# Performance work log

Measured on AMD Instinct MI355X. Metric: run time of the kernel, lower is better.

## Reference

```python
import jax, jax.numpy as jnp
import numpy as np

NGF = 64
EPS = 1e-5


def _rpad(x):
    # ReflectionPad2d(1)
    return jnp.pad(x, ((0, 0), (0, 0), (1, 1), (1, 1)), mode='reflect')


def _inorm(x):
    # InstanceNorm2d(affine=False): per-sample, per-channel over H,W
    m = x.mean(axis=(2, 3), keepdims=True)
    v = ((x - m) ** 2).mean(axis=(2, 3), keepdims=True)
    return (x - m) / jnp.sqrt(v + EPS)


def _pac_conv(xp, gp, w, b):
    # Pixel-adaptive conv (pac.PacConv2d, kernel_type='gaussian', k=3, pad=0).
    # xp: (B,C,H+2,W+2) padded input; gp: (B,Cg,H+2,W+2) padded guide;
    # w: (O,C,3,3), b: (O,)
    B, C, Hp, Wp = xp.shape
    H, W = Hp - 2, Wp - 2
    gc = gp[:, :, 1:1 + H, 1:1 + W]  # guide value at each output pixel (patch center)
    out = jnp.zeros((B, w.shape[0], H, W), xp.dtype)
    for ky in range(3):
        for kx in range(3):
            gs = gp[:, :, ky:ky + H, kx:kx + W]
            # Gaussian adaptive kernel: exp(-0.5 * ||g_nb - g_center||^2), summed over guide channels
            k = jnp.exp(-0.5 * jnp.sum((gs - gc) ** 2, axis=1, keepdims=True))  # (B,1,H,W)
            xs = xp[:, :, ky:ky + H, kx:kx + W] * k
            out = out + jnp.einsum('oc,bchw->bohw', w[:, :, ky, kx], xs)
    return out + b[None, :, None, None]


def _pa_resblock(h, guide, wa, ba, wb, bb):
    gp = _rpad(guide)
    t = h
    h = _pac_conv(_rpad(h), gp, wa, ba)
    h = jax.nn.relu(_inorm(h))
    h = _pac_conv(_rpad(h), gp, wb, bb)
    h = _inorm(h)
    return t + h


def setup_inputs() -> dict:
    key = jax.random.key(0)
    ks = jax.random.split(key, 20)
    B, Cin, H, W = 4, 1, 256, 256
    d = {
        'x': jax.random.normal(ks[0], (B, Cin, H, W), jnp.float32),
        'grad_img': jax.random.normal(ks[1], (B, Cin, H, W), jnp.float32),
        'w0': jax.random.normal(ks[2], (NGF, Cin, 1, 1), jnp.float32) * 0.5,
        'b0': jnp.zeros((NGF,), jnp.float32),
        'wf': jax.random.normal(ks[3], (NGF, NGF, 3, 3), jnp.float32) * 0.05,
        'bf': jnp.zeros((NGF,), jnp.float32),
    }
    for i in (1, 2, 3):
        d[f'w{i}a'] = jax.random.normal(ks[3 + 2 * i], (NGF, NGF, 3, 3), jnp.float32) * 0.05
        d[f'b{i}a'] = jnp.zeros((NGF,), jnp.float32)
        d[f'w{i}b'] = jax.random.normal(ks[4 + 2 * i], (NGF, NGF, 3, 3), jnp.float32) * 0.05
        d[f'b{i}b'] = jnp.zeros((NGF,), jnp.float32)
    return d


def reference(x, grad_img, w0, b0, wf, bf,
              w1a, b1a, w1b, b1b,
              w2a, b2a, w2b, b2b,
              w3a, b3a, w3b, b3b):
    # type == 'ir': y = minmax(grad_img) is computed but unused; guide = x
    guide = x
    # 1x1 stem conv
    h = jnp.einsum('oc,bchw->bohw', w0[:, :, 0, 0], x) + b0[None, :, None, None]
    h = jax.nn.relu(_pa_resblock(h, guide, w1a, b1a, w1b, b1b))
    h = jax.nn.relu(_pa_resblock(h, guide, w2a, b2a, w2b, b2b))
    h = jax.nn.relu(_pa_resblock(h, guide, w3a, b3a, w3b, b3b))
    # model2: reflect pad + 3x3 conv + relu
    hp = _rpad(h)
    out = jax.lax.conv_general_dilated(
        hp, wf, window_strides=(1, 1), padding='VALID',
        dimension_numbers=('NCHW', 'OIHW', 'NCHW'))
    out = jax.nn.relu(out + bf[None, :, None, None])
    return out
```

## Files before the change

kernel.cpp:

```cpp
#include <hip/hip_runtime.h>
#include <hip/hip_bf16.h>
#include <math.h>

#define BN 4
#define CHN 64
#define HH 256
#define WW 256
#define HWSZ (HH*WW)
#define EPSV 1e-5f
#define CP 72

typedef __attribute__((ext_vector_type(8)))  short  short8;
typedef __attribute__((ext_vector_type(4)))  short  short4v;
typedef __attribute__((ext_vector_type(16))) float  floatx16;

__device__ __forceinline__ int refl(int i, int n){ if(i<0)i=-i; if(i>=n)i=2*n-2-i; return i; }
__device__ __forceinline__ short f2bf(float f){ __hip_bfloat16 h=__float2bfloat16(f); return __builtin_bit_cast(short,h); }
__device__ __forceinline__ float bf2f(short s){ unsigned u=((unsigned)(unsigned short)s)<<16; return __builtin_bit_cast(float,u); }

template<int CTRL>
__device__ __forceinline__ float dpp_add(float x){
    int y = __builtin_amdgcn_update_dpp(0, __builtin_bit_cast(int, x), CTRL, 0xF, 0xF, true);
    return x + __builtin_bit_cast(float, y);
}
__device__ __forceinline__ float red_cols(float x){
    x = dpp_add<0xB1>(x);
    x = dpp_add<0x4E>(x);
    x = dpp_add<0x124>(x);
    x = dpp_add<0x128>(x);
    x = dpp_add<0x142>(x);
    return x;
}

__global__ void guide_kernel(const float* __restrict__ x, float* __restrict__ Kb) {
    int idx = blockIdx.x * 256 + threadIdx.x;
    if (idx >= BN*HWSZ) return;
    int b = idx / HWSZ, p = idx - b*HWSZ;
    int y = p / WW, xx = p - y*WW;
    const float* g = x + b*HWSZ;
    float gc = g[p];
#pragma unroll
    for (int t = 0; t < 9; ++t) {
        int yy  = refl(y + t/3 - 1, HH);
        int xx2 = refl(xx + t%3 - 1, WW);
        float d = g[yy*WW + xx2] - gc;
        Kb[(b*9 + t)*HWSZ + p] = __expf(-0.5f*d*d);
    }
}

__global__ void pack_all(const float* w1,const float* w2,const float* w3,const float* w4,
                         const float* w5,const float* w6,const float* w7, short* __restrict__ Ap){
    const float* wsrc[7] = {w1,w2,w3,w4,w5,w6,w7};
    int layer = blockIdx.y;
    int tid = blockIdx.x*256 + threadIdx.x;
    int j    = tid & 7;
    int lane = (tid >> 3) & 63;
    int frag = tid >> 9;
    int oh = frag & 1, cg = (frag >> 1) & 3, t = frag >> 3;
    int o = oh*32 + (lane & 31);
    int c = cg*16 + (lane >> 5)*8 + j;
    Ap[(size_t)layer*36864 + tid] = f2bf(wsrc[layer][(o*CHN + c)*9 + t]);
}

__global__ void conv1x1_kernel(const float* __restrict__ x, const float* __restrict__ w0,
                               const float* __restrict__ b0, short* __restrict__ A){
    int idx = blockIdx.x*256 + threadIdx.x;
    int oc = idx & 7;
    int px = (idx >> 3) % HWSZ;
    int b  = idx / (HWSZ*8);
    float xv = x[(size_t)b*HWSZ + px];
    short8 r;
#pragma unroll
    for (int j = 0; j < 8; ++j) {
        int c = oc*8 + j;
        r[j] = f2bf(fmaf(w0[c], xv, b0[c]));
    }
    *(short8*)(A + ((size_t)(b*HWSZ + px))*64 + oc*8) = r;
}

__global__ void __launch_bounds__(256) reduce_stats(const float* __restrict__ part,
                                                    float* __restrict__ st){
    int b = blockIdx.y, c2 = blockIdx.x;
    const float* p = part + ((size_t)b*1024)*128 + c2;
    int tid = threadIdx.x;
    float s = 0.f;
#pragma unroll
    for (int k = 0; k < 4; ++k) s += p[(size_t)(tid + 256*k)*128];
#pragma unroll
    for (int m = 1; m < 64; m <<= 1) s += __shfl_xor(s, m);
    __shared__ float sm[4];
    if ((tid & 63) == 0) sm[tid >> 6] = s;
    __syncthreads();
    if (tid == 0) st[(size_t)b*128 + c2] = sm[0] + sm[1] + sm[2] + sm[3];
}

template<int NORM, int HASK, int FINAL, int STATS>
__global__ void __launch_bounds__(256, 4) pac_mfma(
    const short* __restrict__ hin, const float* __restrict__ Kb,
    const short* __restrict__ Ap, const float* __restrict__ bias,
    const float* __restrict__ stin, short* __restrict__ outb, float* __restrict__ outf,
    float* __restrict__ stout)
{
    __shared__ short lds[4*34*CP];

    int b  = blockIdx.z;
    int y0 = blockIdx.y * 2;
    int x0 = blockIdx.x * 32;
    int tid = threadIdx.x, lane = tid & 63, wave = tid >> 6;
    int ln2 = lane & 31, hi = lane >> 5, oh = wave & 1, wrow = wave >> 1;
    const short* hb = hin + (size_t)b*HWSZ*64;
    const float* stb = stin + b*64*2;

    float mean[8], rstd[8];
    if (NORM) {
        int c0 = (tid & 7) * 8;
#pragma unroll
        for (int j = 0; j < 8; ++j) {
            float s = stb[(c0+j)*2], s2 = stb[(c0+j)*2+1];
            float m = s * (1.f/HWSZ);
            float var = s2 * (1.f/HWSZ) - m*m;
            mean[j] = m; rstd[j] = rsqrtf(fmaxf(var, 0.f) + EPSV);
        }
    }
#pragma unroll
    for (int it = 0; it < 4; ++it) {
        int chunk = tid + it*256;
        int r = chunk >> 8, o = chunk & 255, px = o >> 3, oc = o & 7;
        int yy = refl(y0 - 1 + r, HH);
        short8 v = *(const short8*)(hb + ((size_t)(yy*WW + x0 + px))*64 + oc*8);
        if (NORM) {
#pragma unroll
            for (int j = 0; j < 8; ++j) {
                float f = bf2f(v[j]);
                f = fmaxf((f - mean[j]) * rstd[j], 0.f);
                v[j] = f2bf(f);
            }
        }
        *(short8*)(lds + (r*34 + 1 + px)*CP + oc*8) = v;
    }
    {
        int r = tid >> 6, c = tid & 63;
        int xm = (x0 == 0) ? 1 : x0 - 1;
        int xp = (x0 + 32 == WW) ? WW - 2 : x0 + 32;
        int yy = refl(y0 - 1 + r, HH);
        float fa = bf2f(hb[((size_t)(yy*WW + xm))*64 + c]);
        float fb = bf2f(hb[((size_t)(yy*WW + xp))*64 + c]);
        if (NORM) {
            float s = stb[c*2], s2 = stb[c*2+1];
            float m = s * (1.f/HWSZ);
            float rs = rsqrtf(fmaxf(s2*(1.f/HWSZ) - m*m, 0.f) + EPSV);
            fa = fmaxf((fa - m)*rs, 0.f);
            fb = fmaxf((fb - m)*rs, 0.f);
        }
        lds[(r*34 + 0)*CP + c]  = f2bf(fa);
        lds[(r*34 + 33)*CP + c] = f2bf(fb);
    }
    __syncthreads();

    float kv[9];
    if (HASK) {
#pragma unroll
        for (int t = 0; t < 9; ++t)
            kv[t] = Kb[((size_t)(b*9 + t))*HWSZ + (y0 + wrow)*WW + x0 + ln2];
    }

    floatx16 acc = (floatx16)(0.f);
    const short8* Ap8 = (const short8*)Ap;
#pragma unroll
    for (int t = 0; t < 9; ++t) {
        int dy = t/3 - 1, dx = t%3 - 1;
        int rr = wrow + dy + 1;
        floatx16 tmp;
#pragma unroll
        for (int cg = 0; cg < 4; ++cg) {
            short8 bf = *(const short8*)(lds + (rr*34 + 1 + ln2 + dx)*CP + cg*16 + hi*8);
            short8 af = Ap8[((size_t)(t*4 + cg)*2 + oh)*64 + lane];
            if (HASK)
                tmp = __builtin_amdgcn_mfma_f32_32x32x16_bf16(af, bf, cg == 0 ? (floatx16)(0.f) : tmp, 0, 0, 0);
            else
                acc = __builtin_amdgcn_mfma_f32_32x32x16_bf16(af, bf, acc, 0, 0, 0);
        }
        if (HASK) {
#pragma unroll
            for (int r = 0; r < 16; ++r) acc[r] = fmaf(kv[t], tmp[r], acc[r]);
        }
    }

#pragma unroll
    for (int q = 0; q < 4; ++q) {
        int o0 = oh*32 + hi*4 + 8*q;
        float4 bq = *(const float4*)(bias + o0);
#pragma unroll
        for (int jj = 0; jj < 4; ++jj) acc[q*4 + jj] += ((float*)&bq)[jj];
    }

    if constexpr (STATS) {
        __shared__ float smst[2][64][2];
        float s[16], s2[16];
#pragma unroll
        for (int r = 0; r < 16; ++r) { float v = acc[r]; s[r] = red_cols(v); s2[r] = red_cols(v*v); }
        if ((lane & 31) == 16) {
#pragma unroll
            for (int r = 0; r < 16; ++r) {
                int o = oh*32 + hi*4 + 8*(r >> 2) + (r & 3);
                smst[wrow][o][0] = s[r];
                smst[wrow][o][1] = s2[r];
            }
        }
        __syncthreads();
        if (tid < 128) {
            int blk = blockIdx.y * gridDim.x + blockIdx.x;
            stout[((size_t)b*1024 + blk)*128 + tid] =
                smst[0][tid >> 1][tid & 1] + smst[1][tid >> 1][tid & 1];
        }
    }

    int y = y0 + wrow, x = x0 + ln2;
#pragma unroll
    for (int q = 0; q < 4; ++q) {
        int o0 = oh*32 + hi*4 + 8*q;
        if (FINAL) {
#pragma unroll
            for (int jj = 0; jj < 4; ++jj) {
                float val = fmaxf(acc[q*4 + jj], 0.f);
                outf[((size_t)(b*64 + o0 + jj))*HWSZ + y*WW + x] = val;
            }
        } else {
            short4v pk;
#pragma unroll
            for (int jj = 0; jj < 4; ++jj) pk[jj] = f2bf(acc[q*4 + jj]);
            *(short4v*)(outb + ((size_t)b*HWSZ + (size_t)(y*WW + x))*64 + o0) = pk;
        }
    }
}

__global__ void addnorm_relu(short* __restrict__ A, const short* __restrict__ C,
                             const float* __restrict__ st){
    int idx = blockIdx.x*256 + threadIdx.x;
    int oc = idx & 7;
    size_t pq = (size_t)(idx >> 3);
    int b = (int)(pq / HWSZ);
    size_t base = pq*64 + oc*8;
    short8 a = *(short8*)(A + base);
    short8 c = *(const short8*)(C + base);
#pragma unroll
    for (int j = 0; j < 8; ++j) {
        int cc = oc*8 + j;
        float s = st[(b*64+cc)*2], s2 = st[(b*64+cc)*2+1];
        float m = s * (1.f/HWSZ);
        float rs = rsqrtf(fmaxf(s2*(1.f/HWSZ) - m*m, 0.f) + EPSV);
        float f = bf2f(a[j]) + (bf2f(c[j]) - m)*rs;
        a[j] = f2bf(fmaxf(f, 0.f));
    }
    *(short8*)(A + base) = a;
}

extern "C" void kernel_launch(void* const* d_in, const int* in_sizes, int n_in,
                              void* d_out, int out_size, void* d_ws, size_t ws_size,
                              hipStream_t stream) {
    const float* x   = (const float*)d_in[0];
    const float* w0  = (const float*)d_in[2];
    const float* b0  = (const float*)d_in[3];
    const float* wf  = (const float*)d_in[4];
    const float* bf  = (const float*)d_in[5];
    const float* w1a = (const float*)d_in[6];  const float* b1a = (const float*)d_in[7];
    const float* w1b = (const float*)d_in[8];  const float* b1b = (const float*)d_in[9];
    const float* w2a = (const float*)d_in[10]; const float* b2a = (const float*)d_in[11];
    const float* w2b = (const float*)d_in[12]; const float* b2b = (const float*)d_in[13];
    const float* w3a = (const float*)d_in[14]; const float* b3a = (const float*)d_in[15];
    const float* w3b = (const float*)d_in[16]; const float* b3b = (const float*)d_in[17];

    float* ws   = (float*)d_ws;
    float* Kb   = ws;
    short* A    = (short*)(Kb + (size_t)BN*9*HWSZ);
    short* Bb   = A + (size_t)BN*HWSZ*64;
    short* Apk  = Bb + (size_t)BN*HWSZ*64;
    float* st   = (float*)(Apk + (size_t)7*36864 + 64);
    float* part = st + 6*BN*64*2;
    short* Cc   = (short*)d_out;

    pack_all<<<dim3(144, 7), 256, 0, stream>>>(w1a, w1b, w2a, w2b, w3a, w3b, wf, Apk);
    guide_kernel<<<(BN*HWSZ + 255)/256, 256, 0, stream>>>(x, Kb);
    conv1x1_kernel<<<BN*HWSZ*8/256, 256, 0, stream>>>(x, w0, b0, A);

    dim3 g(WW/32, HH/2, BN);
    dim3 gr(128, BN);
    const int eblk = BN*HWSZ*8/256;
    const float* biasA[3] = {b1a, b2a, b3a};
    const float* biasB[3] = {b1b, b2b, b3b};

    for (int rb = 0; rb < 3; ++rb) {
        float* stB = st + (size_t)(2*rb)   * BN*64*2;
        float* stC = st + (size_t)(2*rb+1) * BN*64*2;
        pac_mfma<0,1,0,1><<<g, 256, 0, stream>>>(A, Kb, Apk + (size_t)(2*rb)*36864, biasA[rb],
                                                 nullptr, Bb, nullptr, part);
        reduce_stats<<<gr, 256, 0, stream>>>(part, stB);
        pac_mfma<1,1,0,1><<<g, 256, 0, stream>>>(Bb, Kb, Apk + (size_t)(2*rb+1)*36864, biasB[rb],
                                                 stB, Cc, nullptr, part);
        reduce_stats<<<gr, 256, 0, stream>>>(part, stC);
        addnorm_relu<<<eblk, 256, 0, stream>>>(A, Cc, stC);
    }

    pac_mfma<0,0,1,0><<<g, 256, 0, stream>>>(A, Kb, Apk + (size_t)6*36864, bf,
                                             nullptr, nullptr, (float*)d_out, nullptr);
}
```

Before: 474.0 us.

## Fuse residual add-norm-relu into next PAC conv load and merge stem kernels

Removes the standalone addnorm_relu pass by applying the residual add, instance norm and ReLU while the next pac_mfma kernel loads its input tile. The fused kernel writes the new residual to a ping-pong buffer (A/A2) for the following block. The guide-kernel and 1x1 stem conv are merged into one launch. This needs extra workspace, with a fallback to the old path when workspace is too small, and it adds per-tile reads of two tensors in the conv prologue.

```diff
diff --git a/kernel.cpp b/kernel.cpp
--- a/kernel.cpp
+++ b/kernel.cpp
@@ -32,19 +32,31 @@
     return x;
 }
 
-__global__ void guide_kernel(const float* __restrict__ x, float* __restrict__ Kb) {
+__global__ void gc_kernel(const float* __restrict__ x, const float* __restrict__ w0,
+                          const float* __restrict__ b0, float* __restrict__ Kb,
+                          short* __restrict__ A){
     int idx = blockIdx.x * 256 + threadIdx.x;
-    if (idx >= BN*HWSZ) return;
     int b = idx / HWSZ, p = idx - b*HWSZ;
     int y = p / WW, xx = p - y*WW;
-    const float* g = x + b*HWSZ;
+    const float* g = x + (size_t)b*HWSZ;
     float gc = g[p];
 #pragma unroll
     for (int t = 0; t < 9; ++t) {
         int yy  = refl(y + t/3 - 1, HH);
         int xx2 = refl(xx + t%3 - 1, WW);
         float d = g[yy*WW + xx2] - gc;
-        Kb[(b*9 + t)*HWSZ + p] = __expf(-0.5f*d*d);
+        Kb[((size_t)b*9 + t)*HWSZ + p] = __expf(-0.5f*d*d);
+    }
+    short* Ap = A + ((size_t)b*HWSZ + p)*64;
+#pragma unroll
+    for (int oc = 0; oc < 8; ++oc) {
+        short8 r;
+#pragma unroll
+        for (int j = 0; j < 8; ++j) {
+            int c = oc*8 + j;
+            r[j] = f2bf(fmaf(w0[c], gc, b0[c]));
+        }
+        *(short8*)(Ap + oc*8) = r;
     }
 }
 
@@ -62,22 +74,6 @@
     Ap[(size_t)layer*36864 + tid] = f2bf(wsrc[layer][(o*CHN + c)*9 + t]);
 }
 
-__global__ void conv1x1_kernel(const float* __restrict__ x, const float* __restrict__ w0,
-                               const float* __restrict__ b0, short* __restrict__ A){
-    int idx = blockIdx.x*256 + threadIdx.x;
-    int oc = idx & 7;
-    int px = (idx >> 3) % HWSZ;
-    int b  = idx / (HWSZ*8);
-    float xv = x[(size_t)b*HWSZ + px];
-    short8 r;
-#pragma unroll
-    for (int j = 0; j < 8; ++j) {
-        int c = oc*8 + j;
-        r[j] = f2bf(fmaf(w0[c], xv, b0[c]));
-    }
-    *(short8*)(A + ((size_t)(b*HWSZ + px))*64 + oc*8) = r;
-}
-
 __global__ void __launch_bounds__(256) reduce_stats(const float* __restrict__ part,
                                                     float* __restrict__ st){
     int b = blockIdx.y, c2 = blockIdx.x;
@@ -94,14 +90,16 @@
     if (tid == 0) st[(size_t)b*128 + c2] = sm[0] + sm[1] + sm[2] + sm[3];
 }
 
-template<int NORM, int HASK, int FINAL, int STATS>
+template<int NORM, int FUSEA, int WB, int HASK, int FINAL, int STATS>
 __global__ void __launch_bounds__(256, 4) pac_mfma(
-    const short* __restrict__ hin, const float* __restrict__ Kb,
+    const short* __restrict__ hin, const short* __restrict__ cin,
+    const float* __restrict__ Kb,
     const short* __restrict__ Ap, const float* __restrict__ bias,
     const float* __restrict__ stin, short* __restrict__ outb, float* __restrict__ outf,
-    float* __restrict__ stout)
+    short* __restrict__ aout, float* __restrict__ stout)
 {
     __shared__ short lds[4*34*CP];
+    __shared__ float smst[2][64][2];
 
     int b  = blockIdx.z;
     int y0 = blockIdx.y * 2;
@@ -109,10 +107,12 @@
     int tid = threadIdx.x, lane = tid & 63, wave = tid >> 6;
     int ln2 = lane & 31, hi = lane >> 5, oh = wave & 1, wrow = wave >> 1;
     const short* hb = hin + (size_t)b*HWSZ*64;
+    const short* cb = FUSEA ? (cin + (size_t)b*HWSZ*64) : nullptr;
+    short* ab = WB ? (aout + (size_t)b*HWSZ*64) : nullptr;
     const float* stb = stin + b*64*2;
 
     float mean[8], rstd[8];
-    if (NORM) {
+    if (NORM || FUSEA) {
         int c0 = (tid & 7) * 8;
 #pragma unroll
         for (int j = 0; j < 8; ++j) {
@@ -127,7 +127,8 @@
         int chunk = tid + it*256;
         int r = chunk >> 8, o = chunk & 255, px = o >> 3, oc = o & 7;
         int yy = refl(y0 - 1 + r, HH);
-        short8 v = *(const short8*)(hb + ((size_t)(yy*WW + x0 + px))*64 + oc*8);
+        size_t base = ((size_t)(yy*WW + x0 + px))*64 + oc*8;
+        short8 v = *(const short8*)(hb + base);
         if (NORM) {
 #pragma unroll
             for (int j = 0; j < 8; ++j) {
@@ -136,7 +137,18 @@
                 v[j] = f2bf(f);
             }
         }
+        if (FUSEA) {
+            short8 cv = *(const short8*)(cb + base);
+#pragma unroll
+            for (int j = 0; j < 8; ++j) {
+                float f = bf2f(v[j]) + (bf2f(cv[j]) - mean[j]) * rstd[j];
+                v[j] = f2bf(fmaxf(f, 0.f));
+            }
+        }
         *(short8*)(lds + (r*34 + 1 + px)*CP + oc*8) = v;
+        if (WB) {
+            if (r == 1 || r == 2) *(short8*)(ab + base) = v;
+        }
     }
     {
         int r = tid >> 6, c = tid & 63;
@@ -145,12 +157,19 @@
         int yy = refl(y0 - 1 + r, HH);
         float fa = bf2f(hb[((size_t)(yy*WW + xm))*64 + c]);
         float fb = bf2f(hb[((size_t)(yy*WW + xp))*64 + c]);
-        if (NORM) {
+        if (NORM || FUSEA) {
             float s = stb[c*2], s2 = stb[c*2+1];
             float m = s * (1.f/HWSZ);
             float rs = rsqrtf(fmaxf(s2*(1.f/HWSZ) - m*m, 0.f) + EPSV);
-            fa = fmaxf((fa - m)*rs, 0.f);
-            fb = fmaxf((fb - m)*rs, 0.f);
+            if (NORM) {
+                fa = fmaxf((fa - m)*rs, 0.f);
+                fb = fmaxf((fb - m)*rs, 0.f);
+            } else {
+                float fca = bf2f(cb[((size_t)(yy*WW + xm))*64 + c]);
+                float fcb = bf2f(cb[((size_t)(yy*WW + xp))*64 + c]);
+                fa = fmaxf(fa + (fca - m)*rs, 0.f);
+                fb = fmaxf(fb + (fcb - m)*rs, 0.f);
+            }
         }
         lds[(r*34 + 0)*CP + c]  = f2bf(fa);
         lds[(r*34 + 33)*CP + c] = f2bf(fb);
@@ -195,7 +214,6 @@
     }
 
     if constexpr (STATS) {
-        __shared__ float smst[2][64][2];
         float s[16], s2[16];
 #pragma unroll
         for (int r = 0; r < 16; ++r) { float v = acc[r]; s[r] = red_cols(v); s2[r] = red_cols(v*v); }
@@ -270,37 +288,57 @@
     const float* w3a = (const float*)d_in[14]; const float* b3a = (const float*)d_in[15];
     const float* w3b = (const float*)d_in[16]; const float* b3b = (const float*)d_in[17];
 
+    const size_t TEN = (size_t)BN*HWSZ*64;
     float* ws   = (float*)d_ws;
     float* Kb   = ws;
     short* A    = (short*)(Kb + (size_t)BN*9*HWSZ);
-    short* Bb   = A + (size_t)BN*HWSZ*64;
-    short* Apk  = Bb + (size_t)BN*HWSZ*64;
+    short* Bb   = A + TEN;
+    short* Apk  = Bb + TEN;
     float* st   = (float*)(Apk + (size_t)7*36864 + 64);
     float* part = st + 6*BN*64*2;
-    short* Cc   = (short*)d_out;
-
+    short* A2   = (short*)(part + (size_t)BN*1024*128);
+    short* Ccw  = A2 + TEN;
+    size_t need = (size_t)((char*)(Ccw + TEN) - (char*)d_ws);
+    const int FUSED = (ws_size >= need);
+    short* Cc = FUSED ? Ccw : (short*)d_out;
+
+    gc_kernel<<<(BN*HWSZ)/256, 256, 0, stream>>>(x, w0, b0, Kb, A);
     pack_all<<<dim3(144, 7), 256, 0, stream>>>(w1a, w1b, w2a, w2b, w3a, w3b, wf, Apk);
-    guide_kernel<<<(BN*HWSZ + 255)/256, 256, 0, stream>>>(x, Kb);
-    conv1x1_kernel<<<BN*HWSZ*8/256, 256, 0, stream>>>(x, w0, b0, A);
 
     dim3 g(WW/32, HH/2, BN);
     dim3 gr(128, BN);
     const int eblk = BN*HWSZ*8/256;
     const float* biasA[3] = {b1a, b2a, b3a};
     const float* biasB[3] = {b1b, b2b, b3b};
-
+    short* ain[3]  = {A, A, A2};
+    short* awb[3]  = {nullptr, A2, A};
+
+    float* stPrev = nullptr;
     for (int rb = 0; rb < 3; ++rb) {
         float* stB = st + (size_t)(2*rb)   * BN*64*2;
         float* stC = st + (size_t)(2*rb+1) * BN*64*2;
-        pac_mfma<0,1,0,1><<<g, 256, 0, stream>>>(A, Kb, Apk + (size_t)(2*rb)*36864, biasA[rb],
-                                                 nullptr, Bb, nullptr, part);
+        if (FUSED && rb > 0) {
+            pac_mfma<0,1,1,1,0,1><<<g, 256, 0, stream>>>(ain[rb], Cc, Kb,
+                Apk + (size_t)(2*rb)*36864, biasA[rb], stPrev, Bb, nullptr, awb[rb], part);
+        } else {
+            pac_mfma<0,0,0,1,0,1><<<g, 256, 0, stream>>>(ain[FUSED ? rb : 0], nullptr, Kb,
+                Apk + (size_t)(2*rb)*36864, biasA[rb], st , Bb, nullptr, nullptr, part);
+        }
         reduce_stats<<<gr, 256, 0, stream>>>(part, stB);
-        pac_mfma<1,1,0,1><<<g, 256, 0, stream>>>(Bb, Kb, Apk + (size_t)(2*rb+1)*36864, biasB[rb],
-                                                 stB, Cc, nullptr, part);
+        pac_mfma<1,0,0,1,0,1><<<g, 256, 0, stream>>>(Bb, nullptr, Kb,
+            Apk + (size_t)(2*rb+1)*36864, biasB[rb], stB, Cc, nullptr, nullptr, part);
         reduce_stats<<<gr, 256, 0, stream>>>(part, stC);
-        addnorm_relu<<<eblk, 256, 0, stream>>>(A, Cc, stC);
-    }
-
-    pac_mfma<0,0,1,0><<<g, 256, 0, stream>>>(A, Kb, Apk + (size_t)6*36864, bf,
-                                             nullptr, nullptr, (float*)d_out, nullptr);
-}
+        if (!FUSED) {
+            addnorm_relu<<<eblk, 256, 0, stream>>>(A, Cc, stC);
+        }
+        stPrev = stC;
+    }
+
+    if (FUSED) {
+        pac_mfma<0,1,0,0,1,0><<<g, 256, 0, stream>>>(A, Cc, Kb,
+            Apk + (size_t)6*36864, bf, stPrev, nullptr, (float*)d_out, nullptr, nullptr);
+    } else {
+        pac_mfma<0,0,0,0,1,0><<<g, 256, 0, stream>>>(A, nullptr, Kb,
+            Apk + (size_t)6*36864, bf, st , nullptr, (float*)d_out, nullptr, nullptr);
+    }
+}
```

Measured after the change: 468.4 us. Within noise of the previous version (-1.2%).
